# Optimization experiments

Hardware: AMD Instinct MI355X
Metric: run time of the kernel (lower is better)

Reference implementation:

```python
import jax, jax.numpy as jnp
import numpy as np

RNN = 1024
ATT_HID = 512
ATT_FEAT = 2048
ENC = 1024  # input_encoding_size == rnn_size
B = 256
ATT_SIZE = 196


def setup_inputs() -> dict:
    key = jax.random.key(0)
    ks = jax.random.split(key, 9)
    s = lambda fan_in: 1.0 / np.sqrt(fan_in)
    return {
        "h": jax.random.normal(ks[0], (B, RNN), jnp.float32),
        "att_feats": jax.random.normal(ks[1], (B, ATT_SIZE, ATT_FEAT), jnp.float32),
        "p_att_feats": jax.random.normal(ks[2], (B, ATT_SIZE, 2 * ATT_HID), jnp.float32),
        # h2att: Linear(rnn_size, 2*att_hid_size)
        "W_h2att": jax.random.uniform(ks[3], (RNN, 2 * ATT_HID), jnp.float32, -s(RNN), s(RNN)),
        "b_h2att": jax.random.uniform(ks[4], (2 * ATT_HID,), jnp.float32, -s(RNN), s(RNN)),
        # alpha_net: Linear(att_hid_size, 1)
        "w_alpha": jax.random.uniform(ks[5], (ATT_HID,), jnp.float32, -s(ATT_HID), s(ATT_HID)),
        "b_alpha": jax.random.uniform(ks[6], (), jnp.float32, -s(ATT_HID), s(ATT_HID)),
        # att_out: Linear(att_feat_size, 2*input_encoding_size)
        "W_out": jax.random.uniform(ks[7], (ATT_FEAT, 2 * ENC), jnp.float32, -s(ATT_FEAT), s(ATT_FEAT)),
        "b_out": jax.random.uniform(ks[8], (2 * ENC,), jnp.float32, -s(ATT_FEAT), s(ATT_FEAT)),
    }


def reference(h, att_feats, p_att_feats, W_h2att, b_h2att, w_alpha, b_alpha, W_out, b_out):
    # att_h: [B, 2*ATT_HID], broadcast-added over att_size
    att_h = h @ W_h2att + b_h2att
    dot = p_att_feats + att_h[:, None, :]                      # [B, S, 2*H]
    gated = jnp.tanh(dot[..., :ATT_HID]) * jax.nn.sigmoid(dot[..., ATT_HID:])  # [B, S, H]
    scores = jnp.einsum("bsh,h->bs", gated, w_alpha) + b_alpha  # [B, S]
    weight = jax.nn.softmax(scores, axis=-1)                    # [B, S]
    att_res = jnp.einsum("bs,bsf->bf", weight, att_feats)       # [B, ATT_FEAT]
    out = att_res @ W_out + b_out                               # [B, 2*ENC]
    return jnp.tanh(out[:, :RNN]) * jax.nn.sigmoid(out[:, RNN:2 * RNN])  # [B, RNN]
```

## Files before the change

kernel.cpp:

```cpp
#include <hip/hip_runtime.h>

using bf16x8 = __attribute__((ext_vector_type(8))) short;
using f32x4  = __attribute__((ext_vector_type(4))) float;

__device__ __forceinline__ ushort f2bf(float f) {
    union { float f; uint i; } v; v.f = f;
    uint r = v.i + 0x7fffu + ((v.i >> 16) & 1u);
    return (ushort)(r >> 16);
}
__device__ __forceinline__ float gate1(float x1, float x2) {
    float e1 = __expf(2.f * x1);
    float e2 = __expf(-x2);
    return (e1 - 1.f) * __builtin_amdgcn_rcpf((e1 + 1.f) * (1.f + e2));
}

__device__ __forceinline__ void transpose_tile(const float* __restrict__ src,
                                               ushort* __restrict__ dst,
                                               int R, int C, int bx, int by,
                                               float (*t)[33]) {
    int c0 = bx << 5, r0 = by << 5;
    int x = threadIdx.x & 31, y = threadIdx.x >> 5;
#pragma unroll
    for (int j = 0; j < 4; j++)
        t[y + 8 * j][x] = src[(size_t)(r0 + y + 8 * j) * C + c0 + x];
    __syncthreads();
#pragma unroll
    for (int j = 0; j < 4; j++)
        dst[(size_t)(c0 + y + 8 * j) * R + r0 + x] = f2bf(t[x][y + 8 * j]);
}

__global__ __launch_bounds__(256) void k_prep(const float* __restrict__ h,
                                              ushort* __restrict__ hbf,
                                              const float* __restrict__ W1,
                                              ushort* __restrict__ WT1,
                                              const float* __restrict__ W2,
                                              ushort* __restrict__ WT2) {
    __shared__ float t[32][33];
    int bid = blockIdx.x;
    if (bid < 4096) {
        transpose_tile(W2, WT2, 2048, 2048, bid & 63, bid >> 6, t);
    } else if (bid < 4096 + 1024) {
        int r = bid - 4096;
        transpose_tile(W1, WT1, 1024, 1024, r & 31, r >> 5, t);
    } else {
        int r = bid - 5120;
        int i = (r * 256 + threadIdx.x) * 4;
        float4 v = *(const float4*)(h + i);
        uint2 o;
        o.x = (uint)f2bf(v.x) | ((uint)f2bf(v.y) << 16);
        o.y = (uint)f2bf(v.z) | ((uint)f2bf(v.w) << 16);
        *(uint2*)(hbf + i) = o;
    }
}

__global__ __launch_bounds__(256) void k_gemm_bt(const ushort* __restrict__ A,
                                                 const ushort* __restrict__ BT,
                                                 float* __restrict__ Cp,
                                                 int M, int N, int K, int kchunk) {
    __shared__ ushort As[64 * 40];
    __shared__ ushort Bs[64 * 40];
    const int tid = threadIdx.x;
    const int n0 = blockIdx.x << 6, m0 = blockIdx.y << 6;
    const int k0 = blockIdx.z * kchunk;
    const int wave = tid >> 6, lane = tid & 63;
    const int wm = (wave >> 1) << 5, wn = (wave & 1) << 5;
    const int lr = lane & 15, lq = lane >> 4;
    const int srow = tid >> 2, scol = (tid & 3) << 3;

    f32x4 acc00 = {0.f, 0.f, 0.f, 0.f}, acc01 = acc00, acc10 = acc00, acc11 = acc00;
    const ushort* Ap = A + (size_t)(m0 + srow) * K + k0 + scol;
    const ushort* Bp = BT + (size_t)(n0 + srow) * K + k0 + scol;
    ushort* asd = &As[srow * 40 + scol];
    ushort* bsd = &Bs[srow * 40 + scol];

    for (int k = 0; k < kchunk; k += 32) {
        *(uint4*)asd = *(const uint4*)(Ap + k);
        *(uint4*)bsd = *(const uint4*)(Bp + k);
        __syncthreads();
        bf16x8 a0 = *(const bf16x8*)&As[(wm + lr) * 40 + (lq << 3)];
        bf16x8 a1 = *(const bf16x8*)&As[(wm + 16 + lr) * 40 + (lq << 3)];
        bf16x8 b0 = *(const bf16x8*)&Bs[(wn + lr) * 40 + (lq << 3)];
        bf16x8 b1 = *(const bf16x8*)&Bs[(wn + 16 + lr) * 40 + (lq << 3)];
        acc00 = __builtin_amdgcn_mfma_f32_16x16x32_bf16(a0, b0, acc00, 0, 0, 0);
        acc01 = __builtin_amdgcn_mfma_f32_16x16x32_bf16(a0, b1, acc01, 0, 0, 0);
        acc10 = __builtin_amdgcn_mfma_f32_16x16x32_bf16(a1, b0, acc10, 0, 0, 0);
        acc11 = __builtin_amdgcn_mfma_f32_16x16x32_bf16(a1, b1, acc11, 0, 0, 0);
        __syncthreads();
    }
    float* Cb = Cp + (size_t)blockIdx.z * M * N + (size_t)(m0 + wm + lq * 4) * N + n0 + wn + lr;
#pragma unroll
    for (int r = 0; r < 4; r++) {
        Cb[(size_t)r * N]             = acc00[r];
        Cb[(size_t)r * N + 16]        = acc01[r];
        Cb[(size_t)(r + 16) * N]      = acc10[r];
        Cb[(size_t)(r + 16) * N + 16] = acc11[r];
    }
}

__global__ __launch_bounds__(256) void k_reduce_bias(const float* __restrict__ part,
                                                     const float* __restrict__ bias,
                                                     float* __restrict__ outp,
                                                     int MN, int Nmask) {
    int idx = blockIdx.x * 256 + threadIdx.x;
    float s = bias[idx & Nmask];
#pragma unroll
    for (int ks = 0; ks < 4; ks++) s += part[ks * MN + idx];
    outp[idx] = s;
}

__global__ __launch_bounds__(256) void k_scores(const float* __restrict__ p,
                                                const float* __restrict__ att_h,
                                                const float* __restrict__ w_alpha,
                                                const float* __restrict__ b_alpha,
                                                float* __restrict__ scores) {
    int wid = (blockIdx.x << 2) + (threadIdx.x >> 6);
    int lane = threadIdx.x & 63;
    int b = wid / 196;
    const float* pr = p + (size_t)wid * 1024 + lane * 8;
    float4 p1a = *(const float4*)pr;
    float4 p1b = *(const float4*)(pr + 4);
    float4 p2a = *(const float4*)(pr + 512);
    float4 p2b = *(const float4*)(pr + 516);
    const float* ah = att_h + ((size_t)b << 10) + lane * 8;
    float4 a1a = *(const float4*)ah;
    float4 a1b = *(const float4*)(ah + 4);
    float4 a2a = *(const float4*)(ah + 512);
    float4 a2b = *(const float4*)(ah + 516);
    const float* wa = w_alpha + lane * 8;
    float4 w0 = *(const float4*)wa;
    float4 w1 = *(const float4*)(wa + 4);
    float sum = gate1(p1a.x + a1a.x, p2a.x + a2a.x) * w0.x
              + gate1(p1a.y + a1a.y, p2a.y + a2a.y) * w0.y
              + gate1(p1a.z + a1a.z, p2a.z + a2a.z) * w0.z
              + gate1(p1a.w + a1a.w, p2a.w + a2a.w) * w0.w
              + gate1(p1b.x + a1b.x, p2b.x + a2b.x) * w1.x
              + gate1(p1b.y + a1b.y, p2b.y + a2b.y) * w1.y
              + gate1(p1b.z + a1b.z, p2b.z + a2b.z) * w1.z
              + gate1(p1b.w + a1b.w, p2b.w + a2b.w) * w1.w;
#pragma unroll
    for (int off = 32; off; off >>= 1) sum += __shfl_down(sum, off);
    if (lane == 0) scores[wid] = sum + b_alpha[0];
}

__global__ __launch_bounds__(256) void k_attres_sm(const float* __restrict__ feats,
                                                   const float* __restrict__ scores,
                                                   ushort* __restrict__ att_res) {
    int b = blockIdx.x >> 1, fh = blockIdx.x & 1;
    __shared__ float wl[196];
    __shared__ float red[16];
    int t = threadIdx.x;
    float v = (t < 196) ? scores[b * 196 + t] : -3.4e38f;
    float m = v;
#pragma unroll
    for (int off = 32; off; off >>= 1) m = fmaxf(m, __shfl_down(m, off));
    int wv = t >> 6, ln = t & 63;
    if (ln == 0) red[wv] = m;
    __syncthreads();
    if (t == 0) red[8] = fmaxf(fmaxf(red[0], red[1]), fmaxf(red[2], red[3]));
    __syncthreads();
    float M = red[8];
    float e = (t < 196) ? __expf(v - M) : 0.f;
    float s = e;
#pragma unroll
    for (int off = 32; off; off >>= 1) s += __shfl_down(s, off);
    if (ln == 0) red[wv + 4] = s;
    __syncthreads();
    if (t == 0) red[9] = 1.f / (red[4] + red[5] + red[6] + red[7]);
    __syncthreads();
    if (t < 196) wl[t] = e * red[9];
    __syncthreads();
    int f = (fh << 10) + t * 4;
    const float* base = feats + (size_t)b * 196 * 2048 + f;
    float a0 = 0.f, a1 = 0.f, a2 = 0.f, a3 = 0.f;
    for (int s0 = 0; s0 < 196; s0 += 14) {
        float4 q[14];
        float w[14];
#pragma unroll
        for (int j = 0; j < 14; j++) q[j] = *(const float4*)(base + (size_t)(s0 + j) * 2048);
#pragma unroll
        for (int j = 0; j < 14; j++) w[j] = wl[s0 + j];
#pragma unroll
        for (int j = 0; j < 14; j++) {
            a0 += w[j] * q[j].x;
            a1 += w[j] * q[j].y;
            a2 += w[j] * q[j].z;
            a3 += w[j] * q[j].w;
        }
    }
    uint2 o;
    o.x = (uint)f2bf(a0) | ((uint)f2bf(a1) << 16);
    o.y = (uint)f2bf(a2) | ((uint)f2bf(a3) << 16);
    *(uint2*)(att_res + ((size_t)b << 11) + f) = o;
}

__global__ __launch_bounds__(256) void k_gate_out(const float* __restrict__ part,
                                                  const float* __restrict__ b_out,
                                                  float* __restrict__ outp) {
    int idx = blockIdx.x * 256 + threadIdx.x;
    int b = idx >> 10, i = idx & 1023;
    int c1 = (b << 11) + i;
    const int MN = 256 * 2048;
    float o1 = b_out[i];
    float o2 = b_out[i + 1024];
#pragma unroll
    for (int ks = 0; ks < 2; ks++) {
        o1 += part[ks * MN + c1];
        o2 += part[ks * MN + c1 + 1024];
    }
    outp[idx] = gate1(o1, o2);
}

extern "C" void kernel_launch(void* const* d_in, const int* in_sizes, int n_in,
                              void* d_out, int out_size, void* d_ws, size_t ws_size,
                              hipStream_t stream) {
    const float* h         = (const float*)d_in[0];
    const float* att_feats = (const float*)d_in[1];
    const float* p_att     = (const float*)d_in[2];
    const float* W_h2att   = (const float*)d_in[3];
    const float* b_h2att   = (const float*)d_in[4];
    const float* w_alpha   = (const float*)d_in[5];
    const float* b_alpha   = (const float*)d_in[6];
    const float* W_out     = (const float*)d_in[7];
    const float* b_out     = (const float*)d_in[8];
    float* outp = (float*)d_out;

    char* w = (char*)d_ws;
    const size_t KB = 1024;
    ushort* hbf     = (ushort*)w;
    ushort* WT1     = (ushort*)(w + 512 * KB);
    ushort* WT2     = (ushort*)(w + 2560 * KB);
    float*  part1   = (float*)(w + 10752 * KB);
    float*  part5   = (float*)(w + 10752 * KB);
    float*  att_h   = (float*)(w + 14848 * KB);
    float*  scores  = (float*)(w + 15872 * KB);
    ushort* att_res = (ushort*)(w + 16128 * KB);

    k_prep<<<5376, 256, 0, stream>>>(h, hbf, W_h2att, WT1, W_out, WT2);
    k_gemm_bt<<<dim3(16, 4, 4), 256, 0, stream>>>(hbf, WT1, part1, 256, 1024, 1024, 256);
    k_reduce_bias<<<1024, 256, 0, stream>>>(part1, b_h2att, att_h, 256 * 1024, 1023);
    k_scores<<<12544, 256, 0, stream>>>(p_att, att_h, w_alpha, b_alpha, scores);
    k_attres_sm<<<512, 256, 0, stream>>>(att_feats, scores, att_res);
    k_gemm_bt<<<dim3(32, 4, 2), 256, 0, stream>>>(att_res, WT2, part5, 256, 2048, 2048, 1024);
    k_gate_out<<<1024, 256, 0, stream>>>(part5, b_out, outp);
}
```

Measured before the change: 691.6 us.

## Fuse score, softmax and weighted-sum into one per-batch kernel; raise split-K

Merges the score kernel and the softmax/attention-sum kernel into a single 512-thread block per batch row, so scores stay in shared memory and never round-trip through global memory, and one launch disappears. The output GEMM's split-K goes from 2 to 4 to expose more blocks, and the gate kernel now reduces four partial buffers. The fused kernel launches only 256 blocks, which may underuse the GPU while streaming p_att_feats and att_feats, and the extra split-K partials add reduction traffic.

Measured after the change: 691.0 us. About the same (-0.1%).

```diff
diff --git a/kernel.cpp b/kernel.cpp
--- a/kernel.cpp
+++ b/kernel.cpp
@@ -108,19 +108,17 @@
     outp[idx] = s;
 }
 
-__global__ __launch_bounds__(256) void k_scores(const float* __restrict__ p,
-                                                const float* __restrict__ att_h,
-                                                const float* __restrict__ w_alpha,
-                                                const float* __restrict__ b_alpha,
-                                                float* __restrict__ scores) {
-    int wid = (blockIdx.x << 2) + (threadIdx.x >> 6);
-    int lane = threadIdx.x & 63;
-    int b = wid / 196;
-    const float* pr = p + (size_t)wid * 1024 + lane * 8;
-    float4 p1a = *(const float4*)pr;
-    float4 p1b = *(const float4*)(pr + 4);
-    float4 p2a = *(const float4*)(pr + 512);
-    float4 p2b = *(const float4*)(pr + 516);
+__global__ __launch_bounds__(512) void k_att_fused(const float* __restrict__ p,
+                                                   const float* __restrict__ att_h,
+                                                   const float* __restrict__ w_alpha,
+                                                   const float* __restrict__ b_alpha,
+                                                   const float* __restrict__ feats,
+                                                   ushort* __restrict__ att_res) {
+    __shared__ float sc[196];
+    __shared__ float wl[196];
+    const int b = blockIdx.x;
+    const int t = threadIdx.x, wave = t >> 6, lane = t & 63;
+
     const float* ah = att_h + ((size_t)b << 10) + lane * 8;
     float4 a1a = *(const float4*)ah;
     float4 a1b = *(const float4*)(ah + 4);
@@ -129,47 +127,49 @@
     const float* wa = w_alpha + lane * 8;
     float4 w0 = *(const float4*)wa;
     float4 w1 = *(const float4*)(wa + 4);
-    float sum = gate1(p1a.x + a1a.x, p2a.x + a2a.x) * w0.x
-              + gate1(p1a.y + a1a.y, p2a.y + a2a.y) * w0.y
-              + gate1(p1a.z + a1a.z, p2a.z + a2a.z) * w0.z
-              + gate1(p1a.w + a1a.w, p2a.w + a2a.w) * w0.w
-              + gate1(p1b.x + a1b.x, p2b.x + a2b.x) * w1.x
-              + gate1(p1b.y + a1b.y, p2b.y + a2b.y) * w1.y
-              + gate1(p1b.z + a1b.z, p2b.z + a2b.z) * w1.z
-              + gate1(p1b.w + a1b.w, p2b.w + a2b.w) * w1.w;
-#pragma unroll
-    for (int off = 32; off; off >>= 1) sum += __shfl_down(sum, off);
-    if (lane == 0) scores[wid] = sum + b_alpha[0];
-}
-
-__global__ __launch_bounds__(256) void k_attres_sm(const float* __restrict__ feats,
-                                                   const float* __restrict__ scores,
-                                                   ushort* __restrict__ att_res) {
-    int b = blockIdx.x >> 1, fh = blockIdx.x & 1;
-    __shared__ float wl[196];
-    __shared__ float red[16];
-    int t = threadIdx.x;
-    float v = (t < 196) ? scores[b * 196 + t] : -3.4e38f;
-    float m = v;
-#pragma unroll
-    for (int off = 32; off; off >>= 1) m = fmaxf(m, __shfl_down(m, off));
-    int wv = t >> 6, ln = t & 63;
-    if (ln == 0) red[wv] = m;
+    float balpha = b_alpha[0];
+    for (int s = wave; s < 196; s += 8) {
+        const float* pr = p + (((size_t)(b * 196 + s)) << 10) + lane * 8;
+        float4 p1a = *(const float4*)pr;
+        float4 p1b = *(const float4*)(pr + 4);
+        float4 p2a = *(const float4*)(pr + 512);
+        float4 p2b = *(const float4*)(pr + 516);
+        float sum = gate1(p1a.x + a1a.x, p2a.x + a2a.x) * w0.x
+                  + gate1(p1a.y + a1a.y, p2a.y + a2a.y) * w0.y
+                  + gate1(p1a.z + a1a.z, p2a.z + a2a.z) * w0.z
+                  + gate1(p1a.w + a1a.w, p2a.w + a2a.w) * w0.w
+                  + gate1(p1b.x + a1b.x, p2b.x + a2b.x) * w1.x
+                  + gate1(p1b.y + a1b.y, p2b.y + a2b.y) * w1.y
+                  + gate1(p1b.z + a1b.z, p2b.z + a2b.z) * w1.z
+                  + gate1(p1b.w + a1b.w, p2b.w + a2b.w) * w1.w;
+#pragma unroll
+        for (int off = 32; off; off >>= 1) sum += __shfl_down(sum, off);
+        if (lane == 0) sc[s] = sum + balpha;
+    }
     __syncthreads();
-    if (t == 0) red[8] = fmaxf(fmaxf(red[0], red[1]), fmaxf(red[2], red[3]));
+
+    if (wave == 0) {
+        float v0 = (lane < 196) ? sc[lane] : -3.4e38f;
+        float v1 = (lane + 64 < 196) ? sc[lane + 64] : -3.4e38f;
+        float v2 = (lane + 128 < 196) ? sc[lane + 128] : -3.4e38f;
+        float v3 = (lane + 192 < 196) ? sc[lane + 192] : -3.4e38f;
+        float m = fmaxf(fmaxf(v0, v1), fmaxf(v2, v3));
+#pragma unroll
+        for (int off = 32; off; off >>= 1) m = fmaxf(m, __shfl_xor(m, off));
+        float e0 = __expf(v0 - m), e1 = __expf(v1 - m);
+        float e2 = __expf(v2 - m), e3 = __expf(v3 - m);
+        float ssum = e0 + e1 + e2 + e3;
+#pragma unroll
+        for (int off = 32; off; off >>= 1) ssum += __shfl_xor(ssum, off);
+        float inv = 1.f / ssum;
+        if (lane < 196)       wl[lane]       = e0 * inv;
+        if (lane + 64 < 196)  wl[lane + 64]  = e1 * inv;
+        if (lane + 128 < 196) wl[lane + 128] = e2 * inv;
+        if (lane + 192 < 196) wl[lane + 192] = e3 * inv;
+    }
     __syncthreads();
-    float M = red[8];
-    float e = (t < 196) ? __expf(v - M) : 0.f;
-    float s = e;
-#pragma unroll
-    for (int off = 32; off; off >>= 1) s += __shfl_down(s, off);
-    if (ln == 0) red[wv + 4] = s;
-    __syncthreads();
-    if (t == 0) red[9] = 1.f / (red[4] + red[5] + red[6] + red[7]);
-    __syncthreads();
-    if (t < 196) wl[t] = e * red[9];
-    __syncthreads();
-    int f = (fh << 10) + t * 4;
+
+    const int f = t << 2;
     const float* base = feats + (size_t)b * 196 * 2048 + f;
     float a0 = 0.f, a1 = 0.f, a2 = 0.f, a3 = 0.f;
     for (int s0 = 0; s0 < 196; s0 += 14) {
@@ -203,7 +203,7 @@
     float o1 = b_out[i];
     float o2 = b_out[i + 1024];
 #pragma unroll
-    for (int ks = 0; ks < 2; ks++) {
+    for (int ks = 0; ks < 4; ks++) {
         o1 += part[ks * MN + c1];
         o2 += part[ks * MN + c1 + 1024];
     }
@@ -231,15 +231,13 @@
     ushort* WT2     = (ushort*)(w + 2560 * KB);
     float*  part1   = (float*)(w + 10752 * KB);
     float*  part5   = (float*)(w + 10752 * KB);
-    float*  att_h   = (float*)(w + 14848 * KB);
-    float*  scores  = (float*)(w + 15872 * KB);
-    ushort* att_res = (ushort*)(w + 16128 * KB);
+    float*  att_h   = (float*)(w + 18944 * KB);
+    ushort* att_res = (ushort*)(w + 19968 * KB);
 
     k_prep<<<5376, 256, 0, stream>>>(h, hbf, W_h2att, WT1, W_out, WT2);
     k_gemm_bt<<<dim3(16, 4, 4), 256, 0, stream>>>(hbf, WT1, part1, 256, 1024, 1024, 256);
     k_reduce_bias<<<1024, 256, 0, stream>>>(part1, b_h2att, att_h, 256 * 1024, 1023);
-    k_scores<<<12544, 256, 0, stream>>>(p_att, att_h, w_alpha, b_alpha, scores);
-    k_attres_sm<<<512, 256, 0, stream>>>(att_feats, scores, att_res);
-    k_gemm_bt<<<dim3(32, 4, 2), 256, 0, stream>>>(att_res, WT2, part5, 256, 2048, 2048, 1024);
+    k_att_fused<<<256, 512, 0, stream>>>(p_att, att_h, w_alpha, b_alpha, att_feats, att_res);
+    k_gemm_bt<<<dim3(32, 4, 4), 256, 0, stream>>>(att_res, WT2, part5, 256, 2048, 2048, 512);
     k_gate_out<<<1024, 256, 0, stream>>>(part5, b_out, outp);
 }
```
